# Optimization experiments

Hardware: AMD Instinct MI355X
Metric: run time of the kernel (lower is better)

## Reference

```python
import jax, jax.numpy as jnp
import numpy as np

B, S, D, H, SKG = 4, 1024, 1024, 16, 256
HD = D // H  # head dim = 64


def setup_inputs() -> dict:
    key = jax.random.key(0)
    ks = jax.random.split(key, 8)
    std = 0.02
    return {
        "x": jax.random.normal(ks[0], (B, S, D), dtype=jnp.float32),
        "pred_kg": jax.random.normal(ks[1], (B, SKG, D), dtype=jnp.float32),
        "Wc": jax.random.normal(ks[2], (D, 3 * D), dtype=jnp.float32) * std,  # c_attn weight
        "bc": jnp.zeros((3 * D,), dtype=jnp.float32),
        "Wk": jax.random.normal(ks[3], (D, 2 * D), dtype=jnp.float32) * std,  # k_attn weight
        "bk": jnp.zeros((2 * D,), dtype=jnp.float32),
        "Wp": jax.random.normal(ks[4], (D, D), dtype=jnp.float32) * std,     # c_proj weight (shared)
        "bp": jnp.zeros((D,), dtype=jnp.float32),
    }


def _split_heads(t):  # [B, T, D] -> [B, H, T, HD]
    Bb, T, _ = t.shape
    return t.reshape(Bb, T, H, HD).transpose(0, 2, 1, 3)


def _merge_heads(t):  # [B, H, T, HD] -> [B, T, D]
    Bb, _, T, _ = t.shape
    return t.transpose(0, 2, 1, 3).reshape(Bb, T, D)


def reference(x, pred_kg, Wc, bc, Wk, bk, Wp, bp):
    # ---- self-attention branch (GPT-2 style, explicit causal bias blend) ----
    qkv = x @ Wc + bc                       # Conv1D: [B,S,3D]
    q, k, v = jnp.split(qkv, 3, axis=-1)
    q = _split_heads(q)                     # [B,H,S,HD]
    k = _split_heads(k)
    v = _split_heads(v)

    inv_sqrt_d = 1.0 / jnp.sqrt(jnp.float32(HD))
    w = jnp.einsum("bhqd,bhkd->bhqk", q, k) * inv_sqrt_d  # [B,H,S,S]
    causal = jnp.tril(jnp.ones((S, S), dtype=w.dtype))    # bias buffer slice b
    # faithful to: w = w * b - 10000.0 * (1 - b)
    w = w * causal - 10000.0 * (1.0 - causal)
    w = jax.nn.softmax(w, axis=-1)
    a = jnp.einsum("bhqk,bhkd->bhqd", w, v)
    a = _merge_heads(a) @ Wp + bp           # c_proj; resid dropout is identity in eval

    # ---- KG cross-attention branch (shares query and c_proj) ----
    kkv = pred_kg @ Wk + bk                 # [B,SKG,2D]
    kk, kv = jnp.split(kkv, 2, axis=-1)
    kk = _split_heads(kk)                   # [B,H,SKG,HD]
    kv = _split_heads(kv)
    w2 = jnp.einsum("bhqd,bhkd->bhqk", q, kk) * inv_sqrt_d  # [B,H,S,SKG]
    w2 = jax.nn.softmax(w2, axis=-1)
    ka = jnp.einsum("bhqk,bhkd->bhqd", w2, kv)
    ka = _merge_heads(ka) @ Wp + bp

    # concat the two branch outputs along the sequence axis: [B, S+SKG, D]
    return jnp.concatenate([a, ka], axis=1)
```

## Files before the change

### kernel.cpp

```cpp
#include <hip/hip_runtime.h>
#include <hip/hip_bf16.h>

typedef __bf16 bf16_t;
typedef bf16_t bf16x8 __attribute__((ext_vector_type(8)));
typedef bf16_t bf16x4 __attribute__((ext_vector_type(4)));
typedef float f32x4 __attribute__((ext_vector_type(4)));
typedef float f32x16 __attribute__((ext_vector_type(16)));

#define EXP2C 0.1803368867f
#define FEXP2(x) __builtin_amdgcn_exp2f(x)

__device__ __forceinline__ void gload16(const void* g, void* l) {
  __builtin_amdgcn_global_load_lds(
      (const __attribute__((address_space(1))) void*)g,
      (__attribute__((address_space(3))) void*)l, 16, 0, 0);
}

__device__ __forceinline__ unsigned pkbf(float lo, float hi) {
  unsigned short a = __builtin_bit_cast(unsigned short, (bf16_t)lo);
  unsigned short b = __builtin_bit_cast(unsigned short, (bf16_t)hi);
  return (unsigned)a | ((unsigned)b << 16);
}

__device__ __forceinline__ void plswap(unsigned& a, unsigned& b) {
#if __has_builtin(__builtin_amdgcn_permlane32_swap)
  auto r = __builtin_amdgcn_permlane32_swap(a, b, false, false);
  a = r[0]; b = r[1];
#else
  asm("v_permlane32_swap_b32 %0, %1" : "+v"(a), "+v"(b));
#endif
}
__device__ __forceinline__ float xmax32(float x) {
  unsigned a = __builtin_bit_cast(unsigned, x), b = a;
  plswap(a, b);
  return fmaxf(__builtin_bit_cast(float, a), __builtin_bit_cast(float, b));
}
__device__ __forceinline__ float xsum32(float x) {
  unsigned a = __builtin_bit_cast(unsigned, x), b = a;
  plswap(a, b);
  return __builtin_bit_cast(float, a) + __builtin_bit_cast(float, b);
}

__global__ __launch_bounds__(256) void prep_kernel(
    const float* __restrict__ x, bf16_t* __restrict__ xb,
    const float* __restrict__ pkg, bf16_t* __restrict__ pkb,
    const float* __restrict__ Wc, bf16_t* __restrict__ Wct,
    const float* __restrict__ Wk, bf16_t* __restrict__ Wkt,
    const float* __restrict__ Wp, bf16_t* __restrict__ Wpt) {
  __shared__ float tile[32][33];
  const int bid = blockIdx.x, tid = threadIdx.x;
  if (bid < 5120) {
    int i = bid * 256 + tid;
    const float* src; bf16_t* dst;
    if (i < 1048576) { src = x; dst = xb; }
    else { i -= 1048576; src = pkg; dst = pkb; }
    float4 v = reinterpret_cast<const float4*>(src)[i];
    bf16x4 o = { (bf16_t)v.x, (bf16_t)v.y, (bf16_t)v.z, (bf16_t)v.w };
    reinterpret_cast<bf16x4*>(dst)[i] = o;
    return;
  }
  int r = bid - 5120;
  int xx = r % 192, ky = r / 192;
  const float* W; bf16_t* T; int N;
  if (xx < 96) { W = Wc; T = Wct; N = 3072; }
  else if (xx < 160) { W = Wk; T = Wkt; N = 2048; xx -= 96; }
  else { W = Wp; T = Wpt; N = 1024; xx -= 160; }
  const int K = 1024;
  int tx = tid & 31, ty = tid >> 5;
  int n0 = xx * 32, k0 = ky * 32;
#pragma unroll
  for (int i = 0; i < 4; ++i)
    tile[ty + i * 8][tx] = W[(size_t)(k0 + ty + i * 8) * N + n0 + tx];
  __syncthreads();
#pragma unroll
  for (int i = 0; i < 4; ++i)
    T[(size_t)(n0 + ty + i * 8) * K + k0 + tx] = (bf16_t)tile[tx][ty + i * 8];
}

__global__ __launch_bounds__(256) void pack2_kernel(
    const bf16_t* __restrict__ src0, bf16_t* __restrict__ kd0, bf16_t* __restrict__ vd0,
    const bf16_t* __restrict__ src1, bf16_t* __restrict__ kd1, bf16_t* __restrict__ vd1) {
  __shared__ bf16_t vt[32][72];
  const int tid = threadIdx.x;
  int x = blockIdx.x;
  const int bh = blockIdx.y;
  const bf16_t* src; bf16_t *kd, *vd; int R, stride, kcol, vcol, NT, t;
  if (x < 32) { src = src0; kd = kd0; vd = vd0; R = 1024; stride = 3072; kcol = 1024; vcol = 2048; NT = 32; t = x; }
  else        { src = src1; kd = kd1; vd = vd1; R = 256;  stride = 2048; kcol = 0;    vcol = 1024; NT = 8;  t = x - 32; }
  const int b = bh >> 4, h = bh & 15;
  const size_t srow = (size_t)b * R + t * 32;
  const size_t obase = ((size_t)bh * NT + t) * 2048;
  {
    int r = tid >> 3, c = tid & 7;
    bf16x8 d = *(const bf16x8*)&src[(srow + r) * stride + vcol + h * 64 + c * 8];
    *(bf16x8*)&vt[r][c * 8] = d;
  }
  {
    int ks = tid >> 6, l = tid & 63;
    int hi8 = (l >> 5) * 8;
    bf16x8 d = *(const bf16x8*)&src[(srow + (l & 31)) * stride + kcol + h * 64 + ks * 16 + hi8];
    *(bf16x8*)&kd[obase + ks * 512 + l * 8] = d;
  }
  __syncthreads();
  {
    int dd = tid >> 6, l = tid & 63;
    int mb = dd >> 1, ks = dd & 1;
    int hd = mb * 32 + (l & 31);
    int kvr = ks * 16 + (l >> 5) * 8;
    bf16x8 o;
#pragma unroll
    for (int j = 0; j < 8; ++j) o[j] = vt[kvr + j][hd];
    *(bf16x8*)&vd[obase + dd * 512 + l * 8] = o;
  }
}

template <int OUTF32>
__device__ __forceinline__ void gemm_body256(
    bf16_t* sA, bf16_t* sB,
    const bf16_t* __restrict__ A, const bf16_t* __restrict__ Bt,
    const float* __restrict__ bias, void* __restrict__ Cout,
    int N, int K, int bx, int by) {
  const int tid = threadIdx.x;
  const int l = tid & 63, w = tid >> 6;
  const int lr = l & 15, lg = l >> 4;
  const int m0 = by * 256, n0 = bx * 128;
  const int wr = (w >> 1) * 64, wc = (w & 1) * 64;

  const int iA1 = tid + 512;
  const bf16_t* ga0 = A + (size_t)(m0 + (tid >> 2)) * K + (tid & 3) * 8;
  const bf16_t* ga1 = A + (size_t)(m0 + (iA1 >> 2)) * K + (tid & 3) * 8;
  const bf16_t* gb0 = Bt + (size_t)(n0 + (tid >> 2)) * K + (tid & 3) * 8;

  f32x4 acc[4][4] = {};
  const int nk = K >> 5;
  const int HA = 256 * 32, HB = 128 * 32;

  gload16(ga0, &sA[tid * 8]);
  gload16(ga1, &sA[iA1 * 8]);
  gload16(gb0, &sB[tid * 8]);
  __syncthreads();

  int cur = 0;
  for (int kt = 0; kt < nk; ++kt) {
    if (kt + 1 < nk) {
      const int ko = (kt + 1) * 32;
      const int a = (cur ^ 1) * HA, bb = (cur ^ 1) * HB;
      gload16(ga0 + ko, &sA[a + tid * 8]);
      gload16(ga1 + ko, &sA[a + iA1 * 8]);
      gload16(gb0 + ko, &sB[bb + tid * 8]);
    }
    bf16x8 af[4], bv[4];
#pragma unroll
    for (int mf = 0; mf < 4; ++mf)
      af[mf] = *(const bf16x8*)&sA[cur * HA + (wr + mf * 16 + lr) * 32 + lg * 8];
#pragma unroll
    for (int nf = 0; nf < 4; ++nf)
      bv[nf] = *(const bf16x8*)&sB[cur * HB + (wc + nf * 16 + lr) * 32 + lg * 8];
    __builtin_amdgcn_s_setprio(1);
#pragma unroll
    for (int mf = 0; mf < 4; ++mf)
#pragma unroll
      for (int nf = 0; nf < 4; ++nf)
        acc[mf][nf] = __builtin_amdgcn_mfma_f32_16x16x32_bf16(af[mf], bv[nf], acc[mf][nf], 0, 0, 0);
    __builtin_amdgcn_s_setprio(0);
    __syncthreads();
    cur ^= 1;
  }

#pragma unroll
  for (int mf = 0; mf < 4; ++mf) {
#pragma unroll
    for (int nf = 0; nf < 4; ++nf) {
      int col = n0 + wc + nf * 16 + lr;
      float bb = bias[col];
      int rowb = m0 + wr + mf * 16 + lg * 4;
#pragma unroll
      for (int r = 0; r < 4; ++r) {
        float v = acc[mf][nf][r] + bb;
        if constexpr (OUTF32)
          ((float*)Cout)[(size_t)(rowb + r) * N + col] = v;
        else
          ((bf16_t*)Cout)[(size_t)(rowb + r) * N + col] = (bf16_t)v;
      }
    }
  }
}

__global__ __launch_bounds__(512) void gemm2_kernel(
    const bf16_t* __restrict__ A0, const bf16_t* __restrict__ B0,
    const float* __restrict__ bi0, bf16_t* __restrict__ C0,
    const bf16_t* __restrict__ A1, const bf16_t* __restrict__ B1,
    const float* __restrict__ bi1, bf16_t* __restrict__ C1) {
  __shared__ __align__(16) bf16_t sA[2][256 * 32];
  __shared__ __align__(16) bf16_t sB[2][128 * 32];
  int bid = blockIdx.x;
  int wg = (bid & 7) * 56 + (bid >> 3);
  if (wg < 384)
    gemm_body256<0>(&sA[0][0], &sB[0][0], A0, B0, bi0, C0, 3072, 1024, wg % 24, wg / 24);
  else {
    int r = wg - 384;
    gemm_body256<0>(&sA[0][0], &sB[0][0], A1, B1, bi1, C1, 2048, 1024, r % 16, r / 16);
  }
}

__global__ __launch_bounds__(512) void gemm_proj_kernel(
    const bf16_t* __restrict__ A, const bf16_t* __restrict__ Bt,
    const float* __restrict__ bias, float* __restrict__ Cout) {
  __shared__ __align__(16) bf16_t sA[2][256 * 32];
  __shared__ __align__(16) bf16_t sB[2][128 * 32];
  int bid = blockIdx.x;
  int wg = (bid & 7) * 32 + (bid >> 3);
  gemm_body256<1>(&sA[0][0], &sB[0][0], A, Bt, bias, Cout, 1024, 1024, wg % 8, wg / 8);
}

#define STAGE(bf, t)                                                         \
  {                                                                          \
    gload16(kba + (size_t)(t) * 2048 + tid * 8, &sKV[bf][tid * 16]);         \
    gload16(vba + (size_t)(t) * 2048 + tid * 8, &sKV[bf][4096 + tid * 16]);  \
  }
#define QKT()                                                                \
  {                                                                          \
    __builtin_amdgcn_s_setprio(1);                                           \
    _Pragma("unroll") for (int ks = 0; ks < 4; ++ks)                         \
        sa = __builtin_amdgcn_mfma_f32_32x32x16_bf16(kf[ks], qf[ks], sa, 0, 0, 0); \
    __builtin_amdgcn_s_setprio(0);                                           \
  }
#define SMPV(vf, tcur)                                                       \
  {                                                                          \
    float sv[16];                                                            \
    const bool mt = is_self && ((tcur) == qw);                               \
    _Pragma("unroll") for (int r = 0; r < 16; ++r) {                         \
      float v = sa[r];                                                       \
      if (mt) {                                                              \
        int kvr = (r & 3) + 8 * (r >> 2) + kv4;                              \
        v = (kvr > ql) ? -1e30f : v;                                         \
      }                                                                      \
      sv[r] = v;                                                             \
    }                                                                        \
    float tm = fmaxf(                                                        \
        fmaxf(fmaxf(fmaxf(sv[0], sv[1]), fmaxf(sv[2], sv[3])),               \
              fmaxf(fmaxf(sv[4], sv[5]), fmaxf(sv[6], sv[7]))),              \
        fmaxf(fmaxf(fmaxf(sv[8], sv[9]), fmaxf(sv[10], sv[11])),             \
              fmaxf(fmaxf(sv[12], sv[13]), fmaxf(sv[14], sv[15]))));         \
    tm = xmax32(tm);                                                         \
    if (!__all(tm <= mcur + 64.f)) {                                         \
      float mn = fmaxf(mcur, tm);                                            \
      float sc = FEXP2((mcur - mn) * EXP2C);                                 \
      mcur = mn;                                                             \
      lcur *= sc;                                                            \
      _Pragma("unroll") for (int mb = 0; mb < 2; ++mb)                       \
          _Pragma("unroll") for (int r = 0; r < 16; ++r) oacc[mb][r] *= sc;  \
    }                                                                        \
    const float hm = mcur * EXP2C;                                           \
    float pf[16];                                                            \
    _Pragma("unroll") for (int r = 0; r < 16; ++r)                           \
        pf[r] = FEXP2(__builtin_fmaf(sv[r], EXP2C, -hm));                    \
    float ps = (((pf[0] + pf[1]) + (pf[2] + pf[3])) +                        \
                ((pf[4] + pf[5]) + (pf[6] + pf[7]))) +                       \
               (((pf[8] + pf[9]) + (pf[10] + pf[11])) +                      \
                ((pf[12] + pf[13]) + (pf[14] + pf[15])));                    \
    ps = xsum32(ps);                                                         \
    lcur += ps;                                                              \
    unsigned o01 = pkbf(pf[0], pf[1]), o23 = pkbf(pf[2], pf[3]);             \
    unsigned o45 = pkbf(pf[4], pf[5]), o67 = pkbf(pf[6], pf[7]);             \
    unsigned o89 = pkbf(pf[8], pf[9]), o1011 = pkbf(pf[10], pf[11]);         \
    unsigned o1213 = pkbf(pf[12], pf[13]), o1415 = pkbf(pf[14], pf[15]);     \
    plswap(o01, o45); plswap(o23, o67);                                      \
    plswap(o89, o1213); plswap(o1011, o1415);                                \
    uint4 w0 = { o01, o23, o45, o67 };                                       \
    uint4 w1 = { o89, o1011, o1213, o1415 };                                 \
    bf16x8 pb0 = __builtin_bit_cast(bf16x8, w0);                             \
    bf16x8 pb1 = __builtin_bit_cast(bf16x8, w1);                             \
    __builtin_amdgcn_s_setprio(1);                                           \
    oacc[0] = __builtin_amdgcn_mfma_f32_32x32x16_bf16(vf[0], pb0, oacc[0], 0, 0, 0); \
    oacc[0] = __builtin_amdgcn_mfma_f32_32x32x16_bf16(vf[1], pb1, oacc[0], 0, 0, 0); \
    oacc[1] = __builtin_amdgcn_mfma_f32_32x32x16_bf16(vf[2], pb0, oacc[1], 0, 0, 0); \
    oacc[1] = __builtin_amdgcn_mfma_f32_32x32x16_bf16(vf[3], pb1, oacc[1], 0, 0, 0); \
    __builtin_amdgcn_s_setprio(0);                                           \
  }

__global__ __launch_bounds__(256) void attn_kernel(
    const bf16_t* __restrict__ qkv,
    const bf16_t* __restrict__ kfs, const bf16_t* __restrict__ vfs,
    const bf16_t* __restrict__ kfc, const bf16_t* __restrict__ vfc,
    bf16_t* __restrict__ obuf) {
  __shared__ __align__(16) char sKV[2][8192];

  const int tid = threadIdx.x;
  const int w = tid >> 6, l = tid & 63;
  const int ql = l & 31;
  const bool uhi = l >= 32;
  const int kv4 = uhi ? 4 : 0;
  const int hi8 = uhi ? 8 : 0;

  const int bid = blockIdx.x;
  const bool is_self = bid < 512;
  int qb, bh, nt;
  if (is_self) {
    qb = 7 - (bid >> 6);
    bh = bid & 63;
    nt = qb * 4 + 4;
  } else {
    int cb = bid - 512;
    qb = cb >> 6;
    bh = cb & 63;
    nt = 8;
  }
  const int qw = qb * 4 + w;
  const int b = bh >> 4, h = bh & 15;
  const int hcol = h * 64;
  const int q0 = qw * 32;
  const int tlim = is_self ? qw : (nt - 1);

  const bf16_t* kba; const bf16_t* vba; int ooff;
  if (is_self) {
    kba = kfs + (size_t)bh * 32 * 2048; vba = vfs + (size_t)bh * 32 * 2048; ooff = 0;
  } else {
    kba = kfc + (size_t)bh * 8 * 2048;  vba = vfc + (size_t)bh * 8 * 2048;  ooff = 1024;
  }

  const bf16_t* qrow = qkv + (size_t)(b * 1024 + q0 + ql) * 3072 + hcol + hi8;
  bf16x8 qf[4];
#pragma unroll
  for (int ks = 0; ks < 4; ++ks) qf[ks] = *(const bf16x8*)(qrow + ks * 16);

  float mcur = -1e30f, lcur = 0.f;
  f32x16 oacc[2] = {};

  STAGE(0, 0);
  __syncthreads();
  int buf = 0;
  for (int t = 0; t < nt; ++t) {
    if (t + 1 < nt) STAGE(buf ^ 1, t + 1);
    if (t <= tlim) {
      bf16x8 kf[4], vf[4];
#pragma unroll
      for (int c = 0; c < 4; ++c)
        kf[c] = *(const bf16x8*)&sKV[buf][c * 1024 + l * 16];
#pragma unroll
      for (int c = 0; c < 4; ++c)
        vf[c] = *(const bf16x8*)&sKV[buf][4096 + c * 1024 + l * 16];
      f32x16 sa = {};
      QKT();
      SMPV(vf, t);
    }
    __syncthreads();
    buf ^= 1;
  }

  const float rl = 1.0f / lcur;
  char* swp = &sKV[0][0] + w * 4096;
#pragma unroll
  for (int mb = 0; mb < 2; ++mb)
#pragma unroll
    for (int r2 = 0; r2 < 8; ++r2) {
      float lo = oacc[mb][2 * r2] * rl;
      float hiv = oacc[mb][2 * r2 + 1] * rl;
      int hdb = (r2 & 1) * 2 + 8 * (r2 >> 1) + kv4 + mb * 32;
      int off = (ql * 128 + hdb * 2) ^ ((ql & 7) << 4);
      *(unsigned*)(swp + off) = pkbf(lo, hiv);
    }
  __syncthreads();
  const int orow = b * 2048 + ooff + q0;
#pragma unroll
  for (int it = 0; it < 4; ++it) {
    int idx = it * 64 + l;
    int q = idx >> 3, ch = idx & 7;
    int off = (q * 128 + ch * 16) ^ ((q & 7) << 4);
    uint4 d = *(uint4*)(swp + off);
    *(uint4*)&obuf[(size_t)(orow + q) * 1024 + hcol + ch * 8] = d;
  }
}

extern "C" void kernel_launch(void* const* d_in, const int* in_sizes, int n_in,
                              void* d_out, int out_size, void* d_ws, size_t ws_size,
                              hipStream_t stream) {
  (void)in_sizes; (void)n_in; (void)out_size; (void)ws_size;
  const float* x   = (const float*)d_in[0];
  const float* pkg = (const float*)d_in[1];
  const float* Wc  = (const float*)d_in[2];
  const float* bc  = (const float*)d_in[3];
  const float* Wk  = (const float*)d_in[4];
  const float* bk  = (const float*)d_in[5];
  const float* Wp  = (const float*)d_in[6];
  const float* bp  = (const float*)d_in[7];
  float* out = (float*)d_out;

  char* ws = (char*)d_ws;
  const size_t MB = 1u << 20;
  bf16_t* xb   = (bf16_t*)(ws + 0 * MB);
  bf16_t* pkb  = (bf16_t*)(ws + 8 * MB);
  bf16_t* Wct  = (bf16_t*)(ws + 10 * MB);
  bf16_t* Wkt  = (bf16_t*)(ws + 16 * MB);
  bf16_t* Wpt  = (bf16_t*)(ws + 20 * MB);
  bf16_t* kkvb = (bf16_t*)(ws + 22 * MB);
  bf16_t* abuf = (bf16_t*)(ws + 26 * MB);
  bf16_t* vfs  = (bf16_t*)(ws + 0 * MB);
  bf16_t* kfc  = (bf16_t*)(ws + 8 * MB);
  bf16_t* vfc  = (bf16_t*)(ws + 10 * MB);
  bf16_t* qkvb = (bf16_t*)d_out;
  bf16_t* kfs  = (bf16_t*)((char*)d_out + 24 * MB);

  prep_kernel<<<11264, 256, 0, stream>>>(x, xb, pkg, pkb, Wc, Wct, Wk, Wkt, Wp, Wpt);
  gemm2_kernel<<<448, 512, 0, stream>>>(xb, Wct, bc, qkvb, pkb, Wkt, bk, kkvb);
  pack2_kernel<<<dim3(40, 64), 256, 0, stream>>>(qkvb, kfs, vfs, kkvb, kfc, vfc);
  attn_kernel<<<1024, 256, 0, stream>>>(qkvb, kfs, vfs, kfc, vfc, abuf);
  gemm_proj_kernel<<<256, 512, 0, stream>>>(abuf, Wpt, bp, out);
}
```

Before: 123.0 us.

## Rewrite GEMM mainloop with 8-wave ping-pong schedule, swizzled LDS and K=64 tiles

Replaces the double-buffered K=32 GEMM body with a K=64 tile loop that splits each iteration into four MFMA quadrants, interleaving LDS fragment loads and staggered global-to-LDS stages between barriers. LDS rows use an XOR swizzle to avoid bank conflicts, and 96KB of dynamic shared memory holds two stages. Explicit vmcnt/lgkmcnt waits and setprio are meant to overlap memory traffic with MFMA work in both the QKV and projection GEMMs. It forces one workgroup per CU and depends on fragile manual wait counts for correctness.

```diff
diff --git a/kernel.cpp b/kernel.cpp
--- a/kernel.cpp
+++ b/kernel.cpp
@@ -114,10 +114,18 @@
   }
 }
 
+#define MFMA2(mi, ni)                                                         \
+  acc[mi][ni] = __builtin_amdgcn_mfma_f32_16x16x32_bf16(af[(mi) & 1][0], bf[ni][0], acc[mi][ni], 0, 0, 0); \
+  acc[mi][ni] = __builtin_amdgcn_mfma_f32_16x16x32_bf16(af[(mi) & 1][1], bf[ni][1], acc[mi][ni], 0, 0, 0);
+#define MFMA8(qm, qn)                                                         \
+  MFMA2(2 * (qm) + 0, 2 * (qn) + 0) MFMA2(2 * (qm) + 0, 2 * (qn) + 1)         \
+  MFMA2(2 * (qm) + 1, 2 * (qn) + 0) MFMA2(2 * (qm) + 1, 2 * (qn) + 1)
+#define GBAR() __builtin_amdgcn_s_barrier()
+#define LGKM0() asm volatile("s_waitcnt lgkmcnt(0)" ::: "memory")
+
 template <int OUTF32>
-__device__ __forceinline__ void gemm_body256(
-    bf16_t* sA, bf16_t* sB,
-    const bf16_t* __restrict__ A, const bf16_t* __restrict__ Bt,
+__device__ __forceinline__ void gemm8_body(
+    char* smem, const bf16_t* __restrict__ A, const bf16_t* __restrict__ Bt,
     const float* __restrict__ bias, void* __restrict__ Cout,
     int N, int K, int bx, int by) {
   const int tid = threadIdx.x;
@@ -126,45 +134,79 @@
   const int m0 = by * 256, n0 = bx * 128;
   const int wr = (w >> 1) * 64, wc = (w & 1) * 64;
 
-  const int iA1 = tid + 512;
-  const bf16_t* ga0 = A + (size_t)(m0 + (tid >> 2)) * K + (tid & 3) * 8;
-  const bf16_t* ga1 = A + (size_t)(m0 + (iA1 >> 2)) * K + (tid & 3) * 8;
-  const bf16_t* gb0 = Bt + (size_t)(n0 + (tid >> 2)) * K + (tid & 3) * 8;
+  const int sr = tid >> 3;
+  const int scb = ((tid & 7) * 16) ^ ((sr & 7) << 4);
+  const bf16_t* Ab = A + (size_t)m0 * K + (scb >> 1);
+  const bf16_t* Bb = Bt + (size_t)n0 * K + (scb >> 1);
+  const int nk = K >> 6;
+
+  const int hA = w >> 2;
+  const int rA = ((w >> 1) & 1) * 64 + lr;
+  const int rB = wc + lr;
+  const int xr = (lr & 7) << 4;
+
+  auto STAGE_A = [&](int t, int h) {
+    const bf16_t* g = Ab + (size_t)(h * 128 + sr) * K + t * 64;
+    char* d = smem + ((size_t)(t & 1) * 2 + h) * 16384 + tid * 16;
+    gload16(g, d);
+    gload16(g + (size_t)64 * K, d + 8192);
+  };
+  auto STAGE_B = [&](int t) {
+    const bf16_t* g = Bb + (size_t)sr * K + t * 64;
+    char* d = smem + 65536 + (size_t)(t & 1) * 16384 + tid * 16;
+    gload16(g, d);
+    gload16(g + (size_t)64 * K, d + 8192);
+  };
 
   f32x4 acc[4][4] = {};
-  const int nk = K >> 5;
-  const int HA = 256 * 32, HB = 128 * 32;
-
-  gload16(ga0, &sA[tid * 8]);
-  gload16(ga1, &sA[iA1 * 8]);
-  gload16(gb0, &sB[tid * 8]);
-  __syncthreads();
-
-  int cur = 0;
-  for (int kt = 0; kt < nk; ++kt) {
-    if (kt + 1 < nk) {
-      const int ko = (kt + 1) * 32;
-      const int a = (cur ^ 1) * HA, bb = (cur ^ 1) * HB;
-      gload16(ga0 + ko, &sA[a + tid * 8]);
-      gload16(ga1 + ko, &sA[a + iA1 * 8]);
-      gload16(gb0 + ko, &sB[bb + tid * 8]);
-    }
-    bf16x8 af[4], bv[4];
-#pragma unroll
-    for (int mf = 0; mf < 4; ++mf)
-      af[mf] = *(const bf16x8*)&sA[cur * HA + (wr + mf * 16 + lr) * 32 + lg * 8];
-#pragma unroll
-    for (int nf = 0; nf < 4; ++nf)
-      bv[nf] = *(const bf16x8*)&sB[cur * HB + (wc + nf * 16 + lr) * 32 + lg * 8];
+  bf16x8 af[2][2], bf[4][2];
+
+  STAGE_A(0, 0); STAGE_A(0, 1); STAGE_B(0); STAGE_B(1); STAGE_A(1, 0);
+  asm volatile("s_waitcnt vmcnt(4)" ::: "memory");
+  GBAR();
+
+  for (int t = 0; t < nk; ++t) {
+    const char* pA = smem + ((size_t)(t & 1) * 2 + hA) * 16384;
+    const char* pB = smem + 65536 + (size_t)(t & 1) * 16384;
+    auto LDA = [&](int mf, int ks) {
+      return *(const bf16x8*)(pA + (rA + mf * 16) * 128 + ((ks * 64 + lg * 16) ^ xr));
+    };
+    auto LDB = [&](int nf, int ks) {
+      return *(const bf16x8*)(pB + (rB + nf * 16) * 128 + ((ks * 64 + lg * 16) ^ xr));
+    };
+    af[0][0] = LDA(0, 0); af[0][1] = LDA(0, 1);
+    af[1][0] = LDA(1, 0); af[1][1] = LDA(1, 1);
+    bf[0][0] = LDB(0, 0); bf[0][1] = LDB(0, 1);
+    bf[1][0] = LDB(1, 0); bf[1][1] = LDB(1, 1);
+    if (t + 1 < nk) STAGE_A(t + 1, 1);
+    GBAR(); LGKM0();
     __builtin_amdgcn_s_setprio(1);
-#pragma unroll
-    for (int mf = 0; mf < 4; ++mf)
-#pragma unroll
-      for (int nf = 0; nf < 4; ++nf)
-        acc[mf][nf] = __builtin_amdgcn_mfma_f32_16x16x32_bf16(af[mf], bv[nf], acc[mf][nf], 0, 0, 0);
+    MFMA8(0, 0)
     __builtin_amdgcn_s_setprio(0);
-    __syncthreads();
-    cur ^= 1;
+    GBAR();
+    bf[2][0] = LDB(2, 0); bf[2][1] = LDB(2, 1);
+    bf[3][0] = LDB(3, 0); bf[3][1] = LDB(3, 1);
+    GBAR(); LGKM0();
+    __builtin_amdgcn_s_setprio(1);
+    MFMA8(0, 1)
+    __builtin_amdgcn_s_setprio(0);
+    GBAR();
+    af[0][0] = LDA(2, 0); af[0][1] = LDA(2, 1);
+    af[1][0] = LDA(3, 0); af[1][1] = LDA(3, 1);
+    if (t + 2 < nk) STAGE_B(t + 2);
+    GBAR(); LGKM0();
+    __builtin_amdgcn_s_setprio(1);
+    MFMA8(1, 0)
+    __builtin_amdgcn_s_setprio(0);
+    GBAR();
+    if (t + 2 < nk) STAGE_A(t + 2, 0);
+    GBAR();
+    __builtin_amdgcn_s_setprio(1);
+    MFMA8(1, 1)
+    __builtin_amdgcn_s_setprio(0);
+    if (t + 2 < nk)      asm volatile("s_waitcnt vmcnt(4)" ::: "memory");
+    else if (t + 1 < nk) asm volatile("s_waitcnt vmcnt(0)" ::: "memory");
+    GBAR();
   }
 
 #pragma unroll
@@ -186,31 +228,29 @@
   }
 }
 
-__global__ __launch_bounds__(512) void gemm2_kernel(
+__global__ __launch_bounds__(512, 1) void gemm2_kernel(
     const bf16_t* __restrict__ A0, const bf16_t* __restrict__ B0,
     const float* __restrict__ bi0, bf16_t* __restrict__ C0,
     const bf16_t* __restrict__ A1, const bf16_t* __restrict__ B1,
     const float* __restrict__ bi1, bf16_t* __restrict__ C1) {
-  __shared__ __align__(16) bf16_t sA[2][256 * 32];
-  __shared__ __align__(16) bf16_t sB[2][128 * 32];
+  extern __shared__ char smem[];
   int bid = blockIdx.x;
   int wg = (bid & 7) * 56 + (bid >> 3);
   if (wg < 384)
-    gemm_body256<0>(&sA[0][0], &sB[0][0], A0, B0, bi0, C0, 3072, 1024, wg % 24, wg / 24);
+    gemm8_body<0>(smem, A0, B0, bi0, C0, 3072, 1024, wg % 24, wg / 24);
   else {
     int r = wg - 384;
-    gemm_body256<0>(&sA[0][0], &sB[0][0], A1, B1, bi1, C1, 2048, 1024, r % 16, r / 16);
-  }
-}
-
-__global__ __launch_bounds__(512) void gemm_proj_kernel(
+    gemm8_body<0>(smem, A1, B1, bi1, C1, 2048, 1024, r % 16, r / 16);
+  }
+}
+
+__global__ __launch_bounds__(512, 1) void gemm_proj_kernel(
     const bf16_t* __restrict__ A, const bf16_t* __restrict__ Bt,
     const float* __restrict__ bias, float* __restrict__ Cout) {
-  __shared__ __align__(16) bf16_t sA[2][256 * 32];
-  __shared__ __align__(16) bf16_t sB[2][128 * 32];
+  extern __shared__ char smem[];
   int bid = blockIdx.x;
   int wg = (bid & 7) * 32 + (bid >> 3);
-  gemm_body256<1>(&sA[0][0], &sB[0][0], A, Bt, bias, Cout, 1024, 1024, wg % 8, wg / 8);
+  gemm8_body<1>(smem, A, Bt, bias, Cout, 1024, 1024, wg % 8, wg / 8);
 }
 
 #define STAGE(bf, t)                                                         \
@@ -402,8 +442,8 @@
   bf16_t* kfs  = (bf16_t*)((char*)d_out + 24 * MB);
 
   prep_kernel<<<11264, 256, 0, stream>>>(x, xb, pkg, pkb, Wc, Wct, Wk, Wkt, Wp, Wpt);
-  gemm2_kernel<<<448, 512, 0, stream>>>(xb, Wct, bc, qkvb, pkb, Wkt, bk, kkvb);
+  gemm2_kernel<<<448, 512, 98304, stream>>>(xb, Wct, bc, qkvb, pkb, Wkt, bk, kkvb);
   pack2_kernel<<<dim3(40, 64), 256, 0, stream>>>(qkvb, kfs, vfs, kkvb, kfc, vfc);
   attn_kernel<<<1024, 256, 0, stream>>>(qkvb, kfs, vfs, kfc, vfc, abuf);
-  gemm_proj_kernel<<<256, 512, 0, stream>>>(abuf, Wpt, bp, out);
-}
+  gemm_proj_kernel<<<256, 512, 98304, stream>>>(abuf, Wpt, bp, out);
+}
```

New measurement: 112.3 us. 8.7% less time.
